# Performance work log

Measured on AMD Instinct MI355X. Metric: run time of the kernel, lower is better.

The kernel has to match this reference:

```python
import jax, jax.numpy as jnp
import numpy as np

N = 10000   # num_nodes
E = 320000  # num_edges
D = 256     # feature / hidden dim
H = 256


def adj_lap(edge_index, n):
    """Dense normalized adjacency (gcn_norm, no self loops) and sym Laplacian."""
    row, col = edge_index[0], edge_index[1]
    # dense 0/1 adjacency (duplicate edges overwrite with same value, as in the loop)
    A = jnp.zeros((n, n), dtype=jnp.float32).at[row, col].set(1.0)
    # gcn_norm: deg = scatter(w, col) -> column sums
    deg_c = A.sum(axis=0)
    dinv_c = jnp.where(deg_c > 0, jax.lax.rsqrt(jnp.maximum(deg_c, 1e-12)), 0.0)
    anorm = dinv_c[:, None] * A * dinv_c[None, :]
    # get_laplacian 'sym': deg = scatter(w, row) -> row sums; L = I - D^-1/2 A D^-1/2
    deg_r = A.sum(axis=1)
    dinv_r = jnp.where(deg_r > 0, jax.lax.rsqrt(jnp.maximum(deg_r, 1e-12)), 0.0)
    lap = jnp.eye(n, dtype=jnp.float32) - dinv_r[:, None] * A * dinv_r[None, :]
    return lap, anorm


def gcn2(x, M, W1, b1, W2, b2):
    # pretrain_model: two-layer spectral GCN using propagation matrix M
    h = jax.nn.relu(M @ (x @ W1) + b1)
    return M @ (h @ W2) + b2


def setup_inputs() -> dict:
    key = jax.random.key(0)
    k1, k2, k3, k4 = jax.random.split(key, 4)
    x = jax.random.normal(k1, (N, D), dtype=jnp.float32)
    edge_index = jax.random.randint(k2, (2, E), 0, N, dtype=jnp.int64)
    W1 = jax.random.normal(k3, (D, H), dtype=jnp.float32) * 0.05
    b1 = jnp.zeros((H,), dtype=jnp.float32)
    W2 = jax.random.normal(k4, (H, H), dtype=jnp.float32) * 0.05
    b2 = jnp.zeros((H,), dtype=jnp.float32)
    return {"x": x, "edge_index": edge_index, "W1": W1, "b1": b1, "W2": W2, "b2": b2}


def reference(x, edge_index, W1, b1, W2, b2):
    # identity augmentor: x1 = x2 = x, edge_index1 = edge_index2 = edge_index,
    # so adj_lap is identical for both branches (computed once).
    lsym, anorm = adj_lap(edge_index, x.shape[0])
    z1 = gcn2(x, lsym, W1, b1, W2, b2)   # 'high' pass
    z2 = gcn2(x, anorm, W1, b1, W2, b2)  # 'low' pass
    z = z2
    return (z, z1, z2)
```

## Files before the change

kernel.cpp:

```cpp
#include <hip/hip_runtime.h>

#define NN 10000
#define EE 320000
#define HH 256
#define BKT 192

typedef __attribute__((ext_vector_type(8))) short bf16x8;
typedef __attribute__((ext_vector_type(4))) float f32x4;
typedef __attribute__((ext_vector_type(2))) float f32x2;

__device__ float bf2f(unsigned int v) {
    return __uint_as_float(v << 16);
}
__device__ unsigned short f2bf(float f) {
    unsigned int i = __float_as_uint(f);
    return (unsigned short)((i + 0x7fffu + ((i >> 16) & 1u)) >> 16);
}
__device__ unsigned int fp8e(float f) {
    float a = fabsf(f);
    a = fminf(a, 448.0f);
    unsigned int bits = __float_as_uint(a * __uint_as_float(0x03800000u));
    bits = bits + 0x7ffffu + ((bits >> 20) & 1u);
    unsigned int r = bits >> 20;
    if (r > 0x7eu) r = 0x7eu;
    return r | ((__float_as_uint(f) >> 24) & 0x80u);
}
__device__ float fp8d(unsigned int b) {
    float mag = __uint_as_float((b & 0x7fu) << 20) * __uint_as_float(0x7B800000u);
    return __uint_as_float(((b & 0x80u) << 24) | __float_as_uint(mag));
}
__device__ __forceinline__ void fp8dec4(unsigned int g, float* o) {
#if __has_builtin(__builtin_amdgcn_cvt_pk_f32_fp8)
    f32x2 lo = __builtin_amdgcn_cvt_pk_f32_fp8((int)g, false);
    f32x2 hi = __builtin_amdgcn_cvt_pk_f32_fp8((int)g, true);
    o[0] = lo.x; o[1] = lo.y; o[2] = hi.x; o[3] = hi.y;
#else
    #pragma unroll
    for (int j = 0; j < 4; j++) o[j] = fp8d((g >> (8 * j)) & 0xffu);
#endif
}
__device__ __forceinline__ unsigned int fp8e2(float a, float b) {
#if __has_builtin(__builtin_amdgcn_cvt_pk_fp8_f32)
    return (unsigned int)__builtin_amdgcn_cvt_pk_fp8_f32(a, b, 0, false);
#else
    return fp8e(a) | (fp8e(b) << 8);
#endif
}
__device__ unsigned int pk2(unsigned short a, unsigned short b) {
    return (unsigned int)a | ((unsigned int)b << 16);
}
__device__ int eload(const void* ei, int is64, int idx) {
    if (is64) return (int)(((const long long*)ei)[idx]);
    return ((const int*)ei)[idx];
}
__device__ __forceinline__ float dinv_of(int d) {
    return d > 0 ? rsqrtf((float)d) : 0.0f;
}

__global__ void k_AB(const void* x, const void* ei, const void* W1, const void* W2,
                     int* flags, int* rawcnt, unsigned short* bucket,
                     unsigned short* W1sw, unsigned short* W2sw) {
    int b = blockIdx.x, t = threadIdx.x;
    if (b >= 65) {
        __shared__ int s_nz;
        if (t == 0) s_nz = 0;
        __syncthreads();
        if (t < 64) {
            const unsigned int* eu = (const unsigned int*)ei;
            for (int k = t; k < 256; k += 64)
                if (eu[2 * k + 1] != 0) atomicOr(&s_nz, 1);
        }
        __syncthreads();
        int is64 = s_nz ? 0 : 1;
        int e = (b - 65) * 256 + t;
        if (e >= EE) return;
        int r = eload(ei, is64, e);
        int c = eload(ei, is64, EE + e);
        if (r < 0 || r >= NN || c < 0 || c >= NN) return;
        int slot = atomicAdd(&rawcnt[r], 1);
        if (slot < BKT) bucket[(size_t)r * BKT + slot] = (unsigned short)c;
        return;
    }
    if (b == 0) {
        __shared__ int s0, s1;
        if (t == 0) { s0 = 0; s1 = 0; }
        __syncthreads();
        if (t < 64) {
            const unsigned int* eu = (const unsigned int*)ei;
            const unsigned int* xu = (const unsigned int*)x;
            for (int k = t; k < 256; k += 64)
                if (eu[2 * k + 1] != 0) atomicOr(&s0, 1);
            unsigned int lo = xu[t] & 0xffffu;
            unsigned int ex = (lo >> 7) & 0xffu;
            if (lo == 0u || (ex >= 90u && ex <= 150u)) atomicAdd(&s1, 1);
        }
        __syncthreads();
        if (t == 0) {
            flags[0] = s0 ? 0 : 1;
            flags[1] = (s1 >= 56) ? 0 : 1;
        }
        return;
    }
    __shared__ int plaus;
    if (t == 0) plaus = 0;
    __syncthreads();
    if (t < 64) {
        unsigned int lo = ((const unsigned int*)x)[t] & 0xffffu;
        unsigned int ex = (lo >> 7) & 0xffu;
        if (lo == 0u || (ex >= 90u && ex <= 150u)) atomicAdd(&plaus, 1);
    }
    __syncthreads();
    int f32io = (plaus >= 56) ? 0 : 1;
    int vb = b - 1;
    const void* W = (vb < 32) ? W1 : W2;
    unsigned short* O = (vb < 32) ? W1sw : W2sw;
    int g = ((vb < 32) ? vb : vb - 32) * 256 + t;
    int gl = g & 63;
    int n = (g >> 6) & 15;
    int ks = g >> 10;
    int coln = n * 16 + (gl & 15);
    int krow = ks * 32 + ((gl >> 4) & 3) * 8;
    unsigned short v[8];
    if (f32io) {
        const float* Wf = (const float*)W;
        #pragma unroll
        for (int j = 0; j < 8; j++) v[j] = f2bf(Wf[(size_t)(krow + j) * HH + coln]);
    } else {
        const unsigned short* Wh = (const unsigned short*)W;
        #pragma unroll
        for (int j = 0; j < 8; j++) v[j] = Wh[(size_t)(krow + j) * HH + coln];
    }
    uint4 p;
    p.x = pk2(v[0], v[1]); p.y = pk2(v[2], v[3]);
    p.z = pk2(v[4], v[5]); p.w = pk2(v[6], v[7]);
    *(uint4*)(O + (size_t)g * 8) = p;
}

__global__ void k_DG(const void* x, const unsigned short* W1sw, const int* flags,
                     const int* rawcnt, int* cnt2, unsigned short* bucket,
                     unsigned char* Yf8, void* Oout) {
    __shared__ unsigned int bm[4][316];
    __shared__ int cnt[4];
    __shared__ unsigned short As[16][264];
    int b = blockIdx.x;
    int tid = threadIdx.x;
    if (b < 2500) {
        int wave = tid >> 6;
        int lane = tid & 63;
        int i = b * 4 + wave;
        int d = rawcnt[i];
        if (d > BKT) d = BKT;
        for (int t = lane; t < 313; t += 64) bm[wave][t] = 0u;
        if (lane == 0) cnt[wave] = 0;
        unsigned short* bp = bucket + (size_t)i * BKT;
        int cvals[3];
        int nt = 0;
        for (int t = lane; t < d; t += 64) cvals[nt++] = (int)bp[t];
        for (int k = 0; k < nt; k++) {
            int c = cvals[k];
            unsigned int m = 1u << (c & 31);
            unsigned int old = atomicOr(&bm[wave][c >> 5], m);
            if (!(old & m)) {
                int p = atomicAdd(&cnt[wave], 1);
                bp[p] = (unsigned short)c;
                atomicAdd(&cnt2[2 * c + 1], 1);
            }
        }
        if (lane == 0) atomicExch(&cnt2[2 * i], cnt[wave]);
        return;
    }
    int r0 = (b - 2500) * 16;
    int af32 = flags[1];
    {
        int row = tid >> 4, seg = tid & 15;
        if (af32) {
            const float* ap = (const float*)x + (size_t)(r0 + row) * HH + seg * 16;
            unsigned short v[16];
            #pragma unroll
            for (int j = 0; j < 16; j += 4) {
                float4 q = *(const float4*)(ap + j);
                v[j] = f2bf(q.x); v[j + 1] = f2bf(q.y);
                v[j + 2] = f2bf(q.z); v[j + 3] = f2bf(q.w);
            }
            uint4 p0, p1;
            p0.x = pk2(v[0], v[1]);   p0.y = pk2(v[2], v[3]);
            p0.z = pk2(v[4], v[5]);   p0.w = pk2(v[6], v[7]);
            p1.x = pk2(v[8], v[9]);   p1.y = pk2(v[10], v[11]);
            p1.z = pk2(v[12], v[13]); p1.w = pk2(v[14], v[15]);
            *(uint4*)&As[row][seg * 16] = p0;
            *(uint4*)&As[row][seg * 16 + 8] = p1;
        } else {
            const unsigned short* ap = (const unsigned short*)x + (size_t)(r0 + row) * HH + seg * 16;
            *(uint4*)&As[row][seg * 16] = *(const uint4*)ap;
            *(uint4*)&As[row][seg * 16 + 8] = *(const uint4*)(ap + 8);
        }
    }
    __syncthreads();
    int wv = tid >> 6;
    int lane = tid & 63;
    int quad = lane >> 4;
    int l16 = lane & 15;
    f32x4 acc[4] = {{0,0,0,0},{0,0,0,0},{0,0,0,0},{0,0,0,0}};
    for (int ks = 0; ks < 8; ks++) {
        bf16x8 af = *(const bf16x8*)&As[l16][ks * 32 + quad * 8];
        #pragma unroll
        for (int t = 0; t < 4; t++) {
            int n = wv * 4 + t;
            bf16x8 bf = *(const bf16x8*)(W1sw + ((size_t)(ks * 16 + n) * 64 + lane) * 8);
            acc[t] = __builtin_amdgcn_mfma_f32_16x16x32_bf16(af, bf, acc[t], 0, 0, 0);
        }
    }
    size_t chunkW = (size_t)NN * HH;
    #pragma unroll
    for (int t = 0; t < 4; t++) {
        int cn = (wv * 4 + t) * 16 + l16;
        #pragma unroll
        for (int r = 0; r < 4; r += 2) {
            int row = r0 + quad * 4 + r;
            float v0 = acc[t][r], v1 = acc[t][r + 1];
            unsigned int pk = fp8e2(v0, v1);
            size_t idx0 = (size_t)row * HH + cn;
            size_t idx1 = idx0 + HH;
            Yf8[idx0] = (unsigned char)(pk & 0xffu);
            Yf8[idx1] = (unsigned char)((pk >> 8) & 0xffu);
            if (af32) {
                ((float*)Oout)[2 * chunkW + idx0] = v0;
                ((float*)Oout)[2 * chunkW + idx1] = v1;
            } else {
                ((unsigned short*)Oout)[2 * chunkW + idx0] = f2bf(v0);
                ((unsigned short*)Oout)[2 * chunkW + idx1] = f2bf(v1);
            }
        }
    }
}

__global__ __launch_bounds__(512, 4) void k_CD(
        const unsigned char* Yf8, const unsigned short* bucket,
        const int* cnt2, const unsigned short* W2sw, const void* b1,
        const int* flags, unsigned char* G12f8, void* Oout) {
    __shared__ unsigned short Hs[16][264];
    __shared__ float wsc[16];
    int tid = threadIdx.x;
    int wave = tid >> 6;
    int lane = tid & 63;
    int fb = lane * 4;
    int bbase = blockIdx.x * 8;
    int f32io = flags[1];
    size_t chunkW = (size_t)NN * HH;
    float bv[4];
    if (f32io) {
        const float* bp = (const float*)b1 + fb;
        #pragma unroll
        for (int k = 0; k < 4; k++) bv[k] = bp[k];
    } else {
        uint2 br = *(const uint2*)((const unsigned short*)b1 + fb);
        bv[0] = bf2f(br.x & 0xffffu); bv[1] = bf2f(br.x >> 16);
        bv[2] = bf2f(br.y & 0xffffu); bv[3] = bf2f(br.y >> 16);
    }
    {
        int i = bbase + wave;
        float a1[4] = {0, 0, 0, 0};
        float a2[4] = {0, 0, 0, 0};
        int2 ddi = *(const int2*)(cnt2 + 2 * i);
        int n = ddi.x;
        const unsigned short* cp = bucket + (size_t)i * BKT;
        int t = 0;
        for (; t + 8 <= n; t += 8) {
            ushort4 ca = *(const ushort4*)(cp + t);
            ushort4 cb = *(const ushort4*)(cp + t + 4);
            int cx[8] = {(int)ca.x, (int)ca.y, (int)ca.z, (int)ca.w,
                         (int)cb.x, (int)cb.y, (int)cb.z, (int)cb.w};
            unsigned int gv[8];
            #pragma unroll
            for (int j = 0; j < 8; j++)
                gv[j] = *(const unsigned int*)(Yf8 + (size_t)cx[j] * 256 + fb);
            float wx[8], wy[8];
            #pragma unroll
            for (int j = 0; j < 8; j++) {
                int2 dd = *(const int2*)(cnt2 + 2 * cx[j]);
                wx[j] = dinv_of(dd.x);
                wy[j] = dinv_of(dd.y);
            }
            #pragma unroll
            for (int j = 0; j < 8; j++) {
                float y[4];
                fp8dec4(gv[j], y);
                #pragma unroll
                for (int k = 0; k < 4; k++) {
                    a1[k] += wx[j] * y[k];
                    a2[k] += wy[j] * y[k];
                }
            }
        }
        for (; t + 4 <= n; t += 4) {
            ushort4 c4 = *(const ushort4*)(cp + t);
            int cx[4] = {(int)c4.x, (int)c4.y, (int)c4.z, (int)c4.w};
            unsigned int gv[4];
            #pragma unroll
            for (int j = 0; j < 4; j++)
                gv[j] = *(const unsigned int*)(Yf8 + (size_t)cx[j] * 256 + fb);
            float wx[4], wy[4];
            #pragma unroll
            for (int j = 0; j < 4; j++) {
                int2 dd = *(const int2*)(cnt2 + 2 * cx[j]);
                wx[j] = dinv_of(dd.x);
                wy[j] = dinv_of(dd.y);
            }
            #pragma unroll
            for (int j = 0; j < 4; j++) {
                float y[4];
                fp8dec4(gv[j], y);
                #pragma unroll
                for (int k = 0; k < 4; k++) {
                    a1[k] += wx[j] * y[k];
                    a2[k] += wy[j] * y[k];
                }
            }
        }
        for (; t < n; t++) {
            int c = (int)cp[t];
            int2 dd = *(const int2*)(cnt2 + 2 * c);
            float wx = dinv_of(dd.x);
            float wy = dinv_of(dd.y);
            unsigned int g = *(const unsigned int*)(Yf8 + (size_t)c * 256 + fb);
            float y[4];
            fp8dec4(g, y);
            #pragma unroll
            for (int k = 0; k < 4; k++) {
                a1[k] += wx * y[k];
                a2[k] += wy * y[k];
            }
        }
        float wiix = dinv_of(ddi.x);
        float wiiy = dinv_of(ddi.y);
        if (lane == 0) { wsc[wave] = wiix; wsc[8 + wave] = wiiy; }
        float yv[4];
        if (f32io) {
            const float* sp = (const float*)Oout + 2 * chunkW + (size_t)i * HH + fb;
            #pragma unroll
            for (int k = 0; k < 4; k++) yv[k] = sp[k];
        } else {
            uint2 yi = *(const uint2*)((const unsigned short*)Oout + 2 * chunkW + (size_t)i * HH + fb);
            yv[0] = bf2f(yi.x & 0xffffu); yv[1] = bf2f(yi.x >> 16);
            yv[2] = bf2f(yi.y & 0xffffu); yv[3] = bf2f(yi.y >> 16);
        }
        float h1[4], h2[4];
        #pragma unroll
        for (int k = 0; k < 4; k++) {
            h1[k] = fmaxf(0.f, yv[k] - wiix * a1[k] + bv[k]);
            h2[k] = fmaxf(0.f, wiiy * a2[k] + bv[k]);
        }
        uint2 p1, p2;
        p1.x = pk2(f2bf(h1[0]), f2bf(h1[1])); p1.y = pk2(f2bf(h1[2]), f2bf(h1[3]));
        p2.x = pk2(f2bf(h2[0]), f2bf(h2[1])); p2.y = pk2(f2bf(h2[2]), f2bf(h2[3]));
        *(uint2*)&Hs[wave][fb] = p1;
        *(uint2*)&Hs[8 + wave][fb] = p2;
    }
    __syncthreads();
    int quad = lane >> 4;
    int l16 = lane & 15;
    f32x4 acc[2] = {{0,0,0,0},{0,0,0,0}};
    for (int ks = 0; ks < 8; ks++) {
        bf16x8 af = *(const bf16x8*)&Hs[l16][ks * 32 + quad * 8];
        #pragma unroll
        for (int t = 0; t < 2; t++) {
            int n = wave * 2 + t;
            bf16x8 bf = *(const bf16x8*)(W2sw + ((size_t)(ks * 16 + n) * 64 + lane) * 8);
            acc[t] = __builtin_amdgcn_mfma_f32_16x16x32_bf16(af, bf, acc[t], 0, 0, 0);
        }
    }
    #pragma unroll
    for (int t = 0; t < 2; t++) {
        int cn = (wave * 2 + t) * 16 + l16;
        #pragma unroll
        for (int r = 0; r < 4; r += 2) {
            int row16 = quad * 4 + r;
            float v0 = acc[t][r], v1 = acc[t][r + 1];
            if (row16 < 8) {
                int node = bbase + row16;
                unsigned int pk = fp8e2(wsc[row16] * v0, wsc[row16 + 1] * v1);
                G12f8[(size_t)node * 512 + cn] = (unsigned char)(pk & 0xffu);
                G12f8[(size_t)(node + 1) * 512 + cn] = (unsigned char)((pk >> 8) & 0xffu);
                size_t idx0 = (size_t)node * HH + cn;
                size_t idx1 = idx0 + HH;
                if (f32io) {
                    ((float*)Oout)[chunkW + idx0] = v0;
                    ((float*)Oout)[chunkW + idx1] = v1;
                } else {
                    ((unsigned short*)Oout)[chunkW + idx0] = f2bf(v0);
                    ((unsigned short*)Oout)[chunkW + idx1] = f2bf(v1);
                }
            } else {
                int node = bbase + row16 - 8;
                unsigned int pk = fp8e2(wsc[row16] * v0, wsc[row16 + 1] * v1);
                G12f8[(size_t)node * 512 + 256 + cn] = (unsigned char)(pk & 0xffu);
                G12f8[(size_t)(node + 1) * 512 + 256 + cn] = (unsigned char)((pk >> 8) & 0xffu);
            }
        }
    }
}

__global__ __launch_bounds__(256, 4) void k_E(
        const unsigned char* G12f8, const unsigned short* bucket,
        const int* cnt2, const void* bias, const int* flags, void* Oout) {
    int wave = threadIdx.x >> 6;
    int lane = threadIdx.x & 63;
    int half = lane >> 5;
    int sub = lane & 31;
    int fb = sub * 8;
    int goff = half * 256 + fb;
    int i = blockIdx.x * 4 + wave;
    float acc[8] = {0, 0, 0, 0, 0, 0, 0, 0};
    int2 ddi = *(const int2*)(cnt2 + 2 * i);
    int n = ddi.x;
    const unsigned short* cp = bucket + (size_t)i * BKT;
    int t = 0;
    for (; t + 8 <= n; t += 8) {
        ushort4 ca = *(const ushort4*)(cp + t);
        ushort4 cb = *(const ushort4*)(cp + t + 4);
        int cx[8] = {(int)ca.x, (int)ca.y, (int)ca.z, (int)ca.w,
                     (int)cb.x, (int)cb.y, (int)cb.z, (int)cb.w};
        uint2 gv[8];
        #pragma unroll
        for (int j = 0; j < 8; j++)
            gv[j] = *(const uint2*)(G12f8 + (size_t)cx[j] * 512 + goff);
        #pragma unroll
        for (int j = 0; j < 8; j++) {
            float y[4], y2[4];
            fp8dec4(gv[j].x, y);
            fp8dec4(gv[j].y, y2);
            #pragma unroll
            for (int k = 0; k < 4; k++) {
                acc[k]     += y[k];
                acc[4 + k] += y2[k];
            }
        }
    }
    for (; t + 4 <= n; t += 4) {
        ushort4 c4 = *(const ushort4*)(cp + t);
        int cx[4] = {(int)c4.x, (int)c4.y, (int)c4.z, (int)c4.w};
        uint2 gv[4];
        #pragma unroll
        for (int j = 0; j < 4; j++)
            gv[j] = *(const uint2*)(G12f8 + (size_t)cx[j] * 512 + goff);
        #pragma unroll
        for (int j = 0; j < 4; j++) {
            float y[4], y2[4];
            fp8dec4(gv[j].x, y);
            fp8dec4(gv[j].y, y2);
            #pragma unroll
            for (int k = 0; k < 4; k++) {
                acc[k]     += y[k];
                acc[4 + k] += y2[k];
            }
        }
    }
    for (; t < n; t++) {
        int c = (int)cp[t];
        uint2 g = *(const uint2*)(G12f8 + (size_t)c * 512 + goff);
        float y[4], y2[4];
        fp8dec4(g.x, y);
        fp8dec4(g.y, y2);
        #pragma unroll
        for (int k = 0; k < 4; k++) {
            acc[k]     += y[k];
            acc[4 + k] += y2[k];
        }
    }
    int f32io = flags[1];
    float bv[8];
    if (f32io) {
        const float* bp = (const float*)bias + fb;
        #pragma unroll
        for (int k = 0; k < 8; k++) bv[k] = bp[k];
    } else {
        uint4 br = *(const uint4*)((const unsigned short*)bias + fb);
        bv[0] = bf2f(br.x & 0xffffu); bv[1] = bf2f(br.x >> 16);
        bv[2] = bf2f(br.y & 0xffffu); bv[3] = bf2f(br.y >> 16);
        bv[4] = bf2f(br.z & 0xffffu); bv[5] = bf2f(br.z >> 16);
        bv[6] = bf2f(br.w & 0xffffu); bv[7] = bf2f(br.w >> 16);
    }
    size_t base = (size_t)i * HH + fb;
    size_t chunkW = (size_t)NN * HH;
    float z[8];
    if (half == 0) {
        float wiix = dinv_of(ddi.x);
        float gvv[8];
        if (f32io) {
            const float* sp = (const float*)Oout + chunkW + base;
            #pragma unroll
            for (int k = 0; k < 8; k++) gvv[k] = sp[k];
        } else {
            uint4 gi = *(const uint4*)((const unsigned short*)Oout + chunkW + base);
            gvv[0] = bf2f(gi.x & 0xffffu); gvv[1] = bf2f(gi.x >> 16);
            gvv[2] = bf2f(gi.y & 0xffffu); gvv[3] = bf2f(gi.y >> 16);
            gvv[4] = bf2f(gi.z & 0xffffu); gvv[5] = bf2f(gi.z >> 16);
            gvv[6] = bf2f(gi.w & 0xffffu); gvv[7] = bf2f(gi.w >> 16);
        }
        #pragma unroll
        for (int k = 0; k < 8; k++) z[k] = gvv[k] - wiix * acc[k] + bv[k];
        if (f32io) {
            float* o = (float*)Oout + chunkW + base;
            *(float4*)o = make_float4(z[0], z[1], z[2], z[3]);
            *(float4*)(o + 4) = make_float4(z[4], z[5], z[6], z[7]);
        } else {
            uint4 p;
            p.x = pk2(f2bf(z[0]), f2bf(z[1])); p.y = pk2(f2bf(z[2]), f2bf(z[3]));
            p.z = pk2(f2bf(z[4]), f2bf(z[5])); p.w = pk2(f2bf(z[6]), f2bf(z[7]));
            *(uint4*)((unsigned short*)Oout + chunkW + base) = p;
        }
    } else {
        float wiiy = dinv_of(ddi.y);
        #pragma unroll
        for (int k = 0; k < 8; k++) z[k] = wiiy * acc[k] + bv[k];
        if (f32io) {
            float* o0 = (float*)Oout + base;
            float* o2 = (float*)Oout + 2 * chunkW + base;
            float4 pa = make_float4(z[0], z[1], z[2], z[3]);
            float4 pb = make_float4(z[4], z[5], z[6], z[7]);
            *(float4*)o0 = pa; *(float4*)(o0 + 4) = pb;
            *(float4*)o2 = pa; *(float4*)(o2 + 4) = pb;
        } else {
            uint4 p;
            p.x = pk2(f2bf(z[0]), f2bf(z[1])); p.y = pk2(f2bf(z[2]), f2bf(z[3]));
            p.z = pk2(f2bf(z[4]), f2bf(z[5])); p.w = pk2(f2bf(z[6]), f2bf(z[7]));
            *(uint4*)((unsigned short*)Oout + base) = p;
            *(uint4*)((unsigned short*)Oout + 2 * chunkW + base) = p;
        }
    }
}

extern "C" void kernel_launch(void* const* d_in, const int* in_sizes, int n_in,
                              void* d_out, int out_size, void* d_ws, size_t ws_size,
                              hipStream_t stream) {
    const void* x = 0; const void* ei = 0;
    const void* W1 = 0; const void* b1 = 0; const void* W2 = 0; const void* b2 = 0;
    for (int i = 0; i < n_in; i++) {
        int s = in_sizes[i];
        if (s == NN * HH) x = d_in[i];
        else if (s == 2 * EE) ei = d_in[i];
        else if (s == HH * HH) { if (!W1) W1 = d_in[i]; else W2 = d_in[i]; }
        else if (s == HH) { if (!b1) b1 = d_in[i]; else b2 = d_in[i]; }
    }

    char* ws = (char*)d_ws;
    size_t off = 0;
    int* flags = (int*)(ws + off); off += 256;
    int* rawcnt = (int*)(ws + off); off += 40960;
    int* cnt2 = (int*)(ws + off); off += 81920;
    unsigned short* bucket = (unsigned short*)(ws + off); off += (size_t)NN * BKT * 2;
    unsigned short* W1sw = (unsigned short*)(ws + off); off += (size_t)HH * HH * 2;
    unsigned short* W2sw = (unsigned short*)(ws + off); off += (size_t)HH * HH * 2;
    unsigned char* Yf8 = (unsigned char*)(ws + off); off += (size_t)NN * 256;
    unsigned char* G12f8 = (unsigned char*)(ws + off); off += (size_t)NN * 512;

    hipMemsetAsync(rawcnt, 0, 40960 + 81920, stream);
    k_AB<<<65 + EE / 256, 256, 0, stream>>>(x, ei, W1, W2, flags, rawcnt, bucket,
                                            W1sw, W2sw);
    k_DG<<<2500 + 625, 256, 0, stream>>>(x, W1sw, flags, rawcnt, cnt2, bucket,
                                         Yf8, d_out);
    k_CD<<<NN / 8, 512, 0, stream>>>(Yf8, bucket, cnt2, W2sw, b1, flags, G12f8, d_out);
    k_E<<<NN / 4, 256, 0, stream>>>(G12f8, bucket, cnt2, b2, flags, d_out);
}
```

Baseline: 179.3 us.

## Split neighbor gather across two waves per node in CD and E kernels

The sparse aggregation in k_CD and k_E now gives each node two waves. Each wave walks half of the neighbor list, and the partial sums are combined through shared memory behind a barrier. k_CD doubles its block size to 1024 threads, with each wave doing one MFMA column tile instead of two. k_E goes to 512 threads. The aim is more memory-level parallelism and shorter per-wave gather chains on the latency-bound gathers, at the cost of more shared memory, an extra barrier, and lower occupancy caps. __restrict__ qualifiers are also added.

```diff
diff --git a/kernel.cpp b/kernel.cpp
--- a/kernel.cpp
+++ b/kernel.cpp
@@ -136,9 +136,9 @@
     *(uint4*)(O + (size_t)g * 8) = p;
 }
 
-__global__ void k_DG(const void* x, const unsigned short* W1sw, const int* flags,
-                     const int* rawcnt, int* cnt2, unsigned short* bucket,
-                     unsigned char* Yf8, void* Oout) {
+__global__ void k_DG(const void* x, const unsigned short* __restrict__ W1sw,
+                     const int* flags, const int* rawcnt, int* cnt2,
+                     unsigned short* bucket, unsigned char* Yf8, void* Oout) {
     __shared__ unsigned int bm[4][316];
     __shared__ int cnt[4];
     __shared__ unsigned short As[16][264];
@@ -234,106 +234,126 @@
     }
 }
 
-__global__ __launch_bounds__(512, 4) void k_CD(
-        const unsigned char* Yf8, const unsigned short* bucket,
-        const int* cnt2, const unsigned short* W2sw, const void* b1,
-        const int* flags, unsigned char* G12f8, void* Oout) {
+__global__ __launch_bounds__(1024, 2) void k_CD(
+        const unsigned char* __restrict__ Yf8,
+        const unsigned short* __restrict__ bucket,
+        const int* __restrict__ cnt2, const unsigned short* __restrict__ W2sw,
+        const void* __restrict__ b1, const int* __restrict__ flags,
+        unsigned char* G12f8, void* Oout) {
     __shared__ unsigned short Hs[16][264];
+    __shared__ float pp[8][64][8];
     __shared__ float wsc[16];
     int tid = threadIdx.x;
     int wave = tid >> 6;
     int lane = tid & 63;
     int fb = lane * 4;
+    int row = wave >> 1;
+    int half = wave & 1;
     int bbase = blockIdx.x * 8;
     int f32io = flags[1];
     size_t chunkW = (size_t)NN * HH;
-    float bv[4];
-    if (f32io) {
-        const float* bp = (const float*)b1 + fb;
-        #pragma unroll
-        for (int k = 0; k < 4; k++) bv[k] = bp[k];
-    } else {
-        uint2 br = *(const uint2*)((const unsigned short*)b1 + fb);
-        bv[0] = bf2f(br.x & 0xffffu); bv[1] = bf2f(br.x >> 16);
-        bv[2] = bf2f(br.y & 0xffffu); bv[3] = bf2f(br.y >> 16);
-    }
-    {
-        int i = bbase + wave;
-        float a1[4] = {0, 0, 0, 0};
-        float a2[4] = {0, 0, 0, 0};
-        int2 ddi = *(const int2*)(cnt2 + 2 * i);
-        int n = ddi.x;
-        const unsigned short* cp = bucket + (size_t)i * BKT;
-        int t = 0;
-        for (; t + 8 <= n; t += 8) {
-            ushort4 ca = *(const ushort4*)(cp + t);
-            ushort4 cb = *(const ushort4*)(cp + t + 4);
-            int cx[8] = {(int)ca.x, (int)ca.y, (int)ca.z, (int)ca.w,
-                         (int)cb.x, (int)cb.y, (int)cb.z, (int)cb.w};
-            unsigned int gv[8];
-            #pragma unroll
-            for (int j = 0; j < 8; j++)
-                gv[j] = *(const unsigned int*)(Yf8 + (size_t)cx[j] * 256 + fb);
-            float wx[8], wy[8];
-            #pragma unroll
-            for (int j = 0; j < 8; j++) {
-                int2 dd = *(const int2*)(cnt2 + 2 * cx[j]);
-                wx[j] = dinv_of(dd.x);
-                wy[j] = dinv_of(dd.y);
-            }
-            #pragma unroll
-            for (int j = 0; j < 8; j++) {
-                float y[4];
-                fp8dec4(gv[j], y);
-                #pragma unroll
-                for (int k = 0; k < 4; k++) {
-                    a1[k] += wx[j] * y[k];
-                    a2[k] += wy[j] * y[k];
-                }
-            }
-        }
-        for (; t + 4 <= n; t += 4) {
-            ushort4 c4 = *(const ushort4*)(cp + t);
-            int cx[4] = {(int)c4.x, (int)c4.y, (int)c4.z, (int)c4.w};
-            unsigned int gv[4];
-            #pragma unroll
-            for (int j = 0; j < 4; j++)
-                gv[j] = *(const unsigned int*)(Yf8 + (size_t)cx[j] * 256 + fb);
-            float wx[4], wy[4];
-            #pragma unroll
-            for (int j = 0; j < 4; j++) {
-                int2 dd = *(const int2*)(cnt2 + 2 * cx[j]);
-                wx[j] = dinv_of(dd.x);
-                wy[j] = dinv_of(dd.y);
-            }
-            #pragma unroll
-            for (int j = 0; j < 4; j++) {
-                float y[4];
-                fp8dec4(gv[j], y);
-                #pragma unroll
-                for (int k = 0; k < 4; k++) {
-                    a1[k] += wx[j] * y[k];
-                    a2[k] += wy[j] * y[k];
-                }
-            }
-        }
-        for (; t < n; t++) {
-            int c = (int)cp[t];
-            int2 dd = *(const int2*)(cnt2 + 2 * c);
-            float wx = dinv_of(dd.x);
-            float wy = dinv_of(dd.y);
-            unsigned int g = *(const unsigned int*)(Yf8 + (size_t)c * 256 + fb);
+    int i = bbase + row;
+    int2 ddi = *(const int2*)(cnt2 + 2 * i);
+    int n = ddi.x;
+    int nh = (n + 1) >> 1;
+    int t = half ? nh : 0;
+    int tend = half ? n : nh;
+    float a1[4] = {0, 0, 0, 0};
+    float a2[4] = {0, 0, 0, 0};
+    const unsigned short* cp = bucket + (size_t)i * BKT;
+    for (; t + 8 <= tend; t += 8) {
+        ushort4 ca = *(const ushort4*)(cp + t);
+        ushort4 cb = *(const ushort4*)(cp + t + 4);
+        int cx[8] = {(int)ca.x, (int)ca.y, (int)ca.z, (int)ca.w,
+                     (int)cb.x, (int)cb.y, (int)cb.z, (int)cb.w};
+        unsigned int gv[8];
+        #pragma unroll
+        for (int j = 0; j < 8; j++)
+            gv[j] = *(const unsigned int*)(Yf8 + (size_t)cx[j] * 256 + fb);
+        float wx[8], wy[8];
+        #pragma unroll
+        for (int j = 0; j < 8; j++) {
+            int2 dd = *(const int2*)(cnt2 + 2 * cx[j]);
+            wx[j] = dinv_of(dd.x);
+            wy[j] = dinv_of(dd.y);
+        }
+        #pragma unroll
+        for (int j = 0; j < 8; j++) {
             float y[4];
-            fp8dec4(g, y);
+            fp8dec4(gv[j], y);
             #pragma unroll
             for (int k = 0; k < 4; k++) {
-                a1[k] += wx * y[k];
-                a2[k] += wy * y[k];
-            }
+                a1[k] += wx[j] * y[k];
+                a2[k] += wy[j] * y[k];
+            }
+        }
+    }
+    for (; t + 4 <= tend; t += 4) {
+        ushort4 c4 = *(const ushort4*)(cp + t);
+        int cx[4] = {(int)c4.x, (int)c4.y, (int)c4.z, (int)c4.w};
+        unsigned int gv[4];
+        #pragma unroll
+        for (int j = 0; j < 4; j++)
+            gv[j] = *(const unsigned int*)(Yf8 + (size_t)cx[j] * 256 + fb);
+        float wx[4], wy[4];
+        #pragma unroll
+        for (int j = 0; j < 4; j++) {
+            int2 dd = *(const int2*)(cnt2 + 2 * cx[j]);
+            wx[j] = dinv_of(dd.x);
+            wy[j] = dinv_of(dd.y);
+        }
+        #pragma unroll
+        for (int j = 0; j < 4; j++) {
+            float y[4];
+            fp8dec4(gv[j], y);
+            #pragma unroll
+            for (int k = 0; k < 4; k++) {
+                a1[k] += wx[j] * y[k];
+                a2[k] += wy[j] * y[k];
+            }
+        }
+    }
+    for (; t < tend; t++) {
+        int c = (int)cp[t];
+        int2 dd = *(const int2*)(cnt2 + 2 * c);
+        float wx = dinv_of(dd.x);
+        float wy = dinv_of(dd.y);
+        unsigned int g = *(const unsigned int*)(Yf8 + (size_t)c * 256 + fb);
+        float y[4];
+        fp8dec4(g, y);
+        #pragma unroll
+        for (int k = 0; k < 4; k++) {
+            a1[k] += wx * y[k];
+            a2[k] += wy * y[k];
+        }
+    }
+    if (half) {
+        #pragma unroll
+        for (int k = 0; k < 4; k++) {
+            pp[row][lane][k] = a1[k];
+            pp[row][lane][4 + k] = a2[k];
+        }
+    }
+    __syncthreads();
+    if (!half) {
+        #pragma unroll
+        for (int k = 0; k < 4; k++) {
+            a1[k] += pp[row][lane][k];
+            a2[k] += pp[row][lane][4 + k];
+        }
+        float bv[4];
+        if (f32io) {
+            const float* bp = (const float*)b1 + fb;
+            #pragma unroll
+            for (int k = 0; k < 4; k++) bv[k] = bp[k];
+        } else {
+            uint2 br = *(const uint2*)((const unsigned short*)b1 + fb);
+            bv[0] = bf2f(br.x & 0xffffu); bv[1] = bf2f(br.x >> 16);
+            bv[2] = bf2f(br.y & 0xffffu); bv[3] = bf2f(br.y >> 16);
         }
         float wiix = dinv_of(ddi.x);
         float wiiy = dinv_of(ddi.y);
-        if (lane == 0) { wsc[wave] = wiix; wsc[8 + wave] = wiiy; }
+        if (lane == 0) { wsc[row] = wiix; wsc[8 + row] = wiiy; }
         float yv[4];
         if (f32io) {
             const float* sp = (const float*)Oout + 2 * chunkW + (size_t)i * HH + fb;
@@ -353,69 +373,68 @@
         uint2 p1, p2;
         p1.x = pk2(f2bf(h1[0]), f2bf(h1[1])); p1.y = pk2(f2bf(h1[2]), f2bf(h1[3]));
         p2.x = pk2(f2bf(h2[0]), f2bf(h2[1])); p2.y = pk2(f2bf(h2[2]), f2bf(h2[3]));
-        *(uint2*)&Hs[wave][fb] = p1;
-        *(uint2*)&Hs[8 + wave][fb] = p2;
+        *(uint2*)&Hs[row][fb] = p1;
+        *(uint2*)&Hs[8 + row][fb] = p2;
     }
     __syncthreads();
     int quad = lane >> 4;
     int l16 = lane & 15;
-    f32x4 acc[2] = {{0,0,0,0},{0,0,0,0}};
+    f32x4 acc = {0, 0, 0, 0};
     for (int ks = 0; ks < 8; ks++) {
         bf16x8 af = *(const bf16x8*)&Hs[l16][ks * 32 + quad * 8];
-        #pragma unroll
-        for (int t = 0; t < 2; t++) {
-            int n = wave * 2 + t;
-            bf16x8 bf = *(const bf16x8*)(W2sw + ((size_t)(ks * 16 + n) * 64 + lane) * 8);
-            acc[t] = __builtin_amdgcn_mfma_f32_16x16x32_bf16(af, bf, acc[t], 0, 0, 0);
-        }
-    }
+        bf16x8 bf = *(const bf16x8*)(W2sw + ((size_t)(ks * 16 + wave) * 64 + lane) * 8);
+        acc = __builtin_amdgcn_mfma_f32_16x16x32_bf16(af, bf, acc, 0, 0, 0);
+    }
+    int cn = wave * 16 + l16;
     #pragma unroll
-    for (int t = 0; t < 2; t++) {
-        int cn = (wave * 2 + t) * 16 + l16;
-        #pragma unroll
-        for (int r = 0; r < 4; r += 2) {
-            int row16 = quad * 4 + r;
-            float v0 = acc[t][r], v1 = acc[t][r + 1];
-            if (row16 < 8) {
-                int node = bbase + row16;
-                unsigned int pk = fp8e2(wsc[row16] * v0, wsc[row16 + 1] * v1);
-                G12f8[(size_t)node * 512 + cn] = (unsigned char)(pk & 0xffu);
-                G12f8[(size_t)(node + 1) * 512 + cn] = (unsigned char)((pk >> 8) & 0xffu);
-                size_t idx0 = (size_t)node * HH + cn;
-                size_t idx1 = idx0 + HH;
-                if (f32io) {
-                    ((float*)Oout)[chunkW + idx0] = v0;
-                    ((float*)Oout)[chunkW + idx1] = v1;
-                } else {
-                    ((unsigned short*)Oout)[chunkW + idx0] = f2bf(v0);
-                    ((unsigned short*)Oout)[chunkW + idx1] = f2bf(v1);
-                }
+    for (int r = 0; r < 4; r += 2) {
+        int row16 = quad * 4 + r;
+        float v0 = acc[r], v1 = acc[r + 1];
+        unsigned int pk = fp8e2(wsc[row16] * v0, wsc[row16 + 1] * v1);
+        if (row16 < 8) {
+            int node = bbase + row16;
+            G12f8[(size_t)node * 512 + cn] = (unsigned char)(pk & 0xffu);
+            G12f8[(size_t)(node + 1) * 512 + cn] = (unsigned char)((pk >> 8) & 0xffu);
+            size_t idx0 = (size_t)node * HH + cn;
+            size_t idx1 = idx0 + HH;
+            if (f32io) {
+                ((float*)Oout)[chunkW + idx0] = v0;
+                ((float*)Oout)[chunkW + idx1] = v1;
             } else {
-                int node = bbase + row16 - 8;
-                unsigned int pk = fp8e2(wsc[row16] * v0, wsc[row16 + 1] * v1);
-                G12f8[(size_t)node * 512 + 256 + cn] = (unsigned char)(pk & 0xffu);
-                G12f8[(size_t)(node + 1) * 512 + 256 + cn] = (unsigned char)((pk >> 8) & 0xffu);
-            }
-        }
-    }
-}
-
-__global__ __launch_bounds__(256, 4) void k_E(
-        const unsigned char* G12f8, const unsigned short* bucket,
-        const int* cnt2, const void* bias, const int* flags, void* Oout) {
+                ((unsigned short*)Oout)[chunkW + idx0] = f2bf(v0);
+                ((unsigned short*)Oout)[chunkW + idx1] = f2bf(v1);
+            }
+        } else {
+            int node = bbase + row16 - 8;
+            G12f8[(size_t)node * 512 + 256 + cn] = (unsigned char)(pk & 0xffu);
+            G12f8[(size_t)(node + 1) * 512 + 256 + cn] = (unsigned char)((pk >> 8) & 0xffu);
+        }
+    }
+}
+
+__global__ __launch_bounds__(512, 4) void k_E(
+        const unsigned char* __restrict__ G12f8,
+        const unsigned short* __restrict__ bucket,
+        const int* __restrict__ cnt2, const void* __restrict__ bias,
+        const int* __restrict__ flags, void* Oout) {
+    __shared__ float pp[4][64][8];
     int wave = threadIdx.x >> 6;
     int lane = threadIdx.x & 63;
-    int half = lane >> 5;
+    int rowl = wave >> 1;
+    int nhalf = wave & 1;
+    int fhalf = lane >> 5;
     int sub = lane & 31;
     int fb = sub * 8;
-    int goff = half * 256 + fb;
-    int i = blockIdx.x * 4 + wave;
+    int goff = fhalf * 256 + fb;
+    int i = blockIdx.x * 4 + rowl;
     float acc[8] = {0, 0, 0, 0, 0, 0, 0, 0};
     int2 ddi = *(const int2*)(cnt2 + 2 * i);
     int n = ddi.x;
+    int nh = (n + 1) >> 1;
+    int t = nhalf ? nh : 0;
+    int tend = nhalf ? n : nh;
     const unsigned short* cp = bucket + (size_t)i * BKT;
-    int t = 0;
-    for (; t + 8 <= n; t += 8) {
+    for (; t + 8 <= tend; t += 8) {
         ushort4 ca = *(const ushort4*)(cp + t);
         ushort4 cb = *(const ushort4*)(cp + t + 4);
         int cx[8] = {(int)ca.x, (int)ca.y, (int)ca.z, (int)ca.w,
@@ -436,7 +455,7 @@
             }
         }
     }
-    for (; t + 4 <= n; t += 4) {
+    for (; t + 4 <= tend; t += 4) {
         ushort4 c4 = *(const ushort4*)(cp + t);
         int cx[4] = {(int)c4.x, (int)c4.y, (int)c4.z, (int)c4.w};
         uint2 gv[4];
@@ -455,7 +474,7 @@
             }
         }
     }
-    for (; t < n; t++) {
+    for (; t < tend; t++) {
         int c = (int)cp[t];
         uint2 g = *(const uint2*)(G12f8 + (size_t)c * 512 + goff);
         float y[4], y2[4];
@@ -467,6 +486,14 @@
             acc[4 + k] += y2[k];
         }
     }
+    if (nhalf) {
+        #pragma unroll
+        for (int k = 0; k < 8; k++) pp[rowl][lane][k] = acc[k];
+    }
+    __syncthreads();
+    if (nhalf) return;
+    #pragma unroll
+    for (int k = 0; k < 8; k++) acc[k] += pp[rowl][lane][k];
     int f32io = flags[1];
     float bv[8];
     if (f32io) {
@@ -483,7 +510,7 @@
     size_t base = (size_t)i * HH + fb;
     size_t chunkW = (size_t)NN * HH;
     float z[8];
-    if (half == 0) {
+    if (fhalf == 0) {
         float wiix = dinv_of(ddi.x);
         float gvv[8];
         if (f32io) {
@@ -559,6 +586,6 @@
                                             W1sw, W2sw);
     k_DG<<<2500 + 625, 256, 0, stream>>>(x, W1sw, flags, rawcnt, cnt2, bucket,
                                          Yf8, d_out);
-    k_CD<<<NN / 8, 512, 0, stream>>>(Yf8, bucket, cnt2, W2sw, b1, flags, G12f8, d_out);
-    k_E<<<NN / 4, 256, 0, stream>>>(G12f8, bucket, cnt2, b2, flags, d_out);
-}
+    k_CD<<<NN / 8, 1024, 0, stream>>>(Yf8, bucket, cnt2, W2sw, b1, flags, G12f8, d_out);
+    k_E<<<NN / 4, 512, 0, stream>>>(G12f8, bucket, cnt2, b2, flags, d_out);
+}
```

Result: slower. 186.4 us (+3.9%).
